# Optimization experiments

Hardware: AMD Instinct MI355X
Metric: run time of the kernel (lower is better)

## Reference

```python
import jax, jax.numpy as jnp
import numpy as np

G = 10            # int(2 / 0.2) BEV grid side
NUM_PILLARS = G * G
INTERVAL = 0.2
BN_EPS = 1e-5


def setup_inputs() -> dict:
    key = jax.random.key(0)
    ks = jax.random.split(key, 8)
    B, N = 8, 20000
    x = jax.random.normal(ks[0], (B, N, 3), dtype=jnp.float32)
    # Linear weights stored as [in, out] (torch Linear applies x @ W.T); no biases.
    W1 = jax.random.normal(ks[1], (6, 32), dtype=jnp.float32) * 0.1
    W2 = jax.random.normal(ks[2], (32, 64), dtype=jnp.float32) * 0.1
    W3 = jax.random.normal(ks[3], (64, 128), dtype=jnp.float32) * 0.1
    W4 = jax.random.normal(ks[4], (256, 768), dtype=jnp.float32) * 0.05
    bn_gamma = jnp.ones((NUM_PILLARS,), dtype=jnp.float32)
    bn_beta = jnp.zeros((NUM_PILLARS,), dtype=jnp.float32)
    return {"x": x, "W1": W1, "W2": W2, "W3": W3, "W4": W4,
            "bn_gamma": bn_gamma, "bn_beta": bn_beta}


def _encode_sample(p, seg, W1, W2, W3, W4):
    # p: [N,3] swapped coords (Z,Y,X); seg: [N] pillar id in [0,100)
    N = p.shape[0]
    counts = jax.ops.segment_sum(jnp.ones((N,), p.dtype), seg, num_segments=NUM_PILLARS)  # [100]
    cent = jax.ops.segment_sum(p, seg, num_segments=NUM_PILLARS) / jnp.maximum(counts, 1.0)[:, None]
    aug = jnp.concatenate([p, p - cent[seg]], axis=-1)          # [N,6]
    h = jax.nn.relu(aug @ W1)
    h = jax.nn.relu(h @ W2)
    h = jax.nn.relu(h @ W3)                                      # [N,128]
    pil = jax.ops.segment_max(h, seg, num_segments=NUM_PILLARS)  # [100,128] (-inf on empty, never gathered)
    h2 = jnp.concatenate([h, pil[seg]], axis=-1)                 # [N,256]
    h2 = jax.nn.relu(h2 @ W4)                                    # [N,768]
    enc = jax.ops.segment_max(h2, seg, num_segments=NUM_PILLARS) # [100,768]
    return jnp.where(counts[:, None] > 0, enc, 0.0)             # empty pillars stay zero


def reference(x, W1, W2, W3, W4, bn_gamma, bn_beta):
    # column swap [Y,Z,X] -> [Z,Y,X]
    pts = jnp.stack([x[..., 1], x[..., 0], x[..., 2]], axis=-1)  # [B,N,3]
    # pillar indices from (Y, X) = swapped cols 1:3
    yx = jnp.clip(pts[..., 1:] + 1.0, 0.0, 1.99)
    idx = jnp.floor(yx / INTERVAL).astype(jnp.int32)             # trunc == floor (non-negative)
    seg = idx[..., 0] * G + idx[..., 1]                          # [B,N], matches flatten(2) order y*10+x
    feat = jax.vmap(lambda p, s: _encode_sample(p, s, W1, W2, W3, W4))(pts, seg)  # [B,100,768]
    # BatchNorm1d(100) in training mode over [B, 100, 768]: stats over dims (0,2)
    mean = feat.mean(axis=(0, 2))
    var = feat.var(axis=(0, 2))  # biased variance, as torch uses for normalization
    out = (feat - mean[None, :, None]) * jax.lax.rsqrt(var + BN_EPS)[None, :, None]
    return out * bn_gamma[None, :, None] + bn_beta[None, :, None]
```

## Files before the change

### kernel.cpp

```cpp
#include <hip/hip_runtime.h>
#include <stdint.h>

#define B_    8
#define N_    20000
#define NPTS  (B_*N_)
#define G_    10
#define NPIL  100
#define NSB   (B_*NPIL)
#define BN_EPS 1e-5f

#define OFF_COUNTS   0
#define OFF_SUMS     3200
#define OFF_STARTS   12800
#define OFF_ZPAD     16064
#define ZERO_BYTES   16320
#define OFF_CENT     19264
#define OFF_SEG      28864
#define OFF_W3BF     668864
#define OFF_W4T      709824
#define OFF_PILBF    1103040
#define OFF_PILW4B   1307840
#define OFF_H3P      3765440
#define WS_NEED      44725440

typedef __attribute__((ext_vector_type(8))) short bf16x8;
typedef __attribute__((ext_vector_type(4))) float f32x4;

typedef const __attribute__((address_space(1))) void gas_void;
typedef __attribute__((address_space(3))) void las_void;

__device__ __forceinline__ void gload_lds16(const void* g, void* l){
    __builtin_amdgcn_global_load_lds((gas_void*)g, (las_void*)l, 16, 0, 0);
}

__device__ __forceinline__ int binidx(float v){
    float t = v + 1.0f;
    t = fminf(fmaxf(t, 0.0f), 1.99f);
    return (int)(t / 0.2f);
}
__device__ __forceinline__ unsigned short f2bf(float f){
    unsigned u = __float_as_uint(f);
    u += 0x7fffu + ((u >> 16) & 1u);
    return (unsigned short)(u >> 16);
}
__device__ __forceinline__ unsigned u16max2(unsigned a, unsigned b){
    unsigned ah=a>>16, bh=b>>16, al=a&0xffffu, bl=b&0xffffu;
    return ((ah>bh?ah:bh)<<16) | (al>bl?al:bl);
}
__device__ __forceinline__ uint4 max16(uint4 a, uint4 b){
    uint4 r; r.x=u16max2(a.x,b.x); r.y=u16max2(a.y,b.y);
    r.z=u16max2(a.z,b.z); r.w=u16max2(a.w,b.w); return r;
}

__global__ __launch_bounds__(256) void kA(const float* __restrict__ x,
                                          int* __restrict__ segrank,
                                          int* __restrict__ counts,
                                          float* __restrict__ sums){
    __shared__ int   lc[NSB];
    __shared__ float lsum[NSB*3];
    __shared__ int   lbase[NSB];
    int tid = threadIdx.x;
    for (int j = tid; j < NSB; j += 256){
        lc[j] = 0;
        lsum[3*j] = 0.f; lsum[3*j+1] = 0.f; lsum[3*j+2] = 0.f;
    }
    __syncthreads();
    int i0 = blockIdx.x * 625;
    int sbv[3], lrv[3];
    #pragma unroll
    for (int t = 0; t < 3; t++){
        int i = i0 + tid + t*256;
        sbv[t] = -1;
        if (tid + t*256 < 625 && i < NPTS){
            float x0 = x[3*i], x1 = x[3*i+1], x2 = x[3*i+2];
            int b  = i / N_;
            int sb = b*NPIL + binidx(x0)*G_ + binidx(x2);
            sbv[t] = sb;
            lrv[t] = atomicAdd(&lc[sb], 1);
            atomicAdd(&lsum[sb*3+0], x1);
            atomicAdd(&lsum[sb*3+1], x0);
            atomicAdd(&lsum[sb*3+2], x2);
        }
    }
    __syncthreads();
    for (int j = tid; j < NSB; j += 256){
        int c = lc[j];
        if (c > 0){
            lbase[j] = atomicAdd(&counts[j], c);
            atomicAdd(&sums[3*j+0], lsum[3*j+0]);
            atomicAdd(&sums[3*j+1], lsum[3*j+1]);
            atomicAdd(&sums[3*j+2], lsum[3*j+2]);
        }
    }
    __syncthreads();
    #pragma unroll
    for (int t = 0; t < 3; t++){
        if (sbv[t] >= 0){
            int i = i0 + tid + t*256;
            int rank = lbase[sbv[t]] + lrv[t];
            segrank[i] = sbv[t] | (rank << 10);
        }
    }
}

__global__ __launch_bounds__(1024) void kScan(const int* __restrict__ counts,
                                              int* __restrict__ starts){
    __shared__ int s[1024];
    int t = threadIdx.x;
    int c = (t < NSB) ? counts[t] : 0;
    s[t] = c;
    __syncthreads();
    for (int off=1; off<1024; off<<=1){
        int v = (t >= off) ? s[t-off] : 0;
        __syncthreads();
        s[t] += v;
        __syncthreads();
    }
    if (t < NSB) starts[t] = s[t]-c;
    if (t == NSB) starts[NSB] = s[NSB-1];
}

__global__ __launch_bounds__(256) void kB(const int* __restrict__ counts,
                                          const float* __restrict__ sums,
                                          float* __restrict__ cent,
                                          const float* __restrict__ W3,
                                          unsigned short* __restrict__ W3bf,
                                          const float* __restrict__ W4,
                                          unsigned short* __restrict__ W4T){
    int idx = blockIdx.x*256 + threadIdx.x;
    if (idx < 2400){
        cent[idx] = sums[idx] / fmaxf((float)counts[idx/3], 1.0f);
    } else if (idx < 2400 + 8192){
        int t = idx - 2400;
        int col = t >> 6, k = t & 63;
        W3bf[t] = f2bf(W3[k*128 + col]);
    } else if (idx < 2400 + 8192 + 196608){
        int t = idx - 2400 - 8192;
        int k = t / 768, j = t - k*768;
        W4T[j*256 + k] = f2bf(W4[t]);
    }
}

__global__ __launch_bounds__(256) void kC12(const float* __restrict__ x,
                                            const int* __restrict__ segrank,
                                            const int* __restrict__ starts,
                                            const float* __restrict__ cent,
                                            const float* __restrict__ W1,
                                            const float* __restrict__ W2,
                                            unsigned short* __restrict__ h3p){
    int i = blockIdx.x*256 + threadIdx.x;
    if (i >= NPTS) return;
    int pk = segrank[i];
    int sb = pk & 1023;
    int pos = starts[sb] + (pk >> 10);
    float p0 = x[3*i+1], p1 = x[3*i], p2 = x[3*i+2];
    float aug[6];
    aug[0]=p0; aug[1]=p1; aug[2]=p2;
    aug[3]=p0-cent[sb*3+0]; aug[4]=p1-cent[sb*3+1]; aug[5]=p2-cent[sb*3+2];

    float h1[32];
    #pragma unroll
    for (int j=0;j<32;j++){
        float a = 0.f;
        #pragma unroll
        for (int k=0;k<6;k++) a += aug[k]*W1[k*32+j];
        h1[j] = fmaxf(a, 0.f);
    }
    unsigned buf[32];
    #pragma unroll 8
    for (int jp=0;jp<32;jp++){
        float a0 = 0.f, a1 = 0.f;
        #pragma unroll
        for (int k=0;k<32;k++){
            a0 += h1[k]*W2[k*64 + jp*2];
            a1 += h1[k]*W2[k*64 + jp*2 + 1];
        }
        buf[jp] = (unsigned)f2bf(fmaxf(a0,0.f)) | ((unsigned)f2bf(fmaxf(a1,0.f)) << 16);
    }
    uint4* d4 = (uint4*)(h3p + (size_t)pos*128 + 64);
    #pragma unroll
    for (int q=0;q<8;q++) d4[q] = ((const uint4*)buf)[q];
}

__global__ __launch_bounds__(512) void kC3(const unsigned short* __restrict__ W3bf,
                                           unsigned short* __restrict__ h3p){
    __shared__ unsigned short Al[256*64];
    __shared__ unsigned short Bl[128*64];
    int tid = threadIdx.x;
    int m0  = blockIdx.x * 256;
    #pragma unroll
    for (int it=0; it<4; it++){
        int cc = tid + it*512;
        int row = cc >> 3, ch = cc & 7;
        int chs = ch ^ (row & 7);
        gload_lds16(h3p + (size_t)(m0+row)*128 + 64 + chs*8, (char*)Al + cc*16);
    }
    #pragma unroll
    for (int it=0; it<2; it++){
        int cc = tid + it*512;
        int row = cc >> 3, ch = cc & 7;
        int chs = ch ^ (row & 7);
        gload_lds16(W3bf + (size_t)row*64 + chs*8, (char*)Bl + cc*16);
    }
    __syncthreads();

    int lane = tid & 63, wid = tid >> 6;
    int wm = wid >> 1, wn = wid & 1;
    int l15 = lane & 15, lhi = lane >> 4;

    f32x4 acc[4][4];
    #pragma unroll
    for (int m=0;m<4;m++)
        #pragma unroll
        for (int n=0;n<4;n++) acc[m][n] = (f32x4){0.f,0.f,0.f,0.f};

    #pragma unroll
    for (int kk=0; kk<2; kk++){
        bf16x8 af[4], bfr[4];
        #pragma unroll
        for (int f=0; f<4; f++){
            int ra = wm*64 + f*16 + l15;
            af[f]  = *(const bf16x8*)((char*)Al + ra*128 + (((kk*4+lhi) ^ (ra&7))*16));
            int rb = wn*64 + f*16 + l15;
            bfr[f] = *(const bf16x8*)((char*)Bl + rb*128 + (((kk*4+lhi) ^ (rb&7))*16));
        }
        #pragma unroll
        for (int m=0;m<4;m++)
            #pragma unroll
            for (int n=0;n<4;n++)
                acc[m][n] = __builtin_amdgcn_mfma_f32_16x16x32_bf16(af[m], bfr[n], acc[m][n], 0,0,0);
    }

    #pragma unroll
    for (int m=0;m<4;m++)
        #pragma unroll
        for (int r=0;r<4;r++){
            int row = m0 + wm*64 + m*16 + lhi*4 + r;
            #pragma unroll
            for (int n=0;n<4;n++){
                int col = wn*64 + n*16 + l15;
                h3p[(size_t)row*128 + col] = f2bf(fmaxf(acc[m][n][r], 0.f));
            }
        }
}

__global__ __launch_bounds__(256) void kM(const unsigned short* __restrict__ h3p,
                                          const int* __restrict__ starts,
                                          unsigned short* __restrict__ pilbf){
    __shared__ uint4 sd[16][16];
    int sb = blockIdx.x;
    int tx = threadIdx.x & 15, ty = threadIdx.x >> 4;
    int s = starts[sb], npts = starts[sb+1] - s;
    uint4 acc = {0u,0u,0u,0u};
    for (int p = ty; p < npts; p += 16){
        uint4 v = *(const uint4*)(h3p + (size_t)(s+p)*128 + tx*8);
        acc = max16(acc, v);
    }
    sd[ty][tx] = acc;
    __syncthreads();
    #pragma unroll
    for (int off=8; off; off>>=1){
        if (ty < off) sd[ty][tx] = max16(sd[ty][tx], sd[ty+off][tx]);
        __syncthreads();
    }
    if (ty == 0) *(uint4*)(pilbf + sb*128 + tx*8) = sd[0][tx];
}

__global__ __launch_bounds__(256) void kPB(const unsigned short* __restrict__ pilbf,
                                           const unsigned short* __restrict__ W4T,
                                           float* __restrict__ pilW4b){
    __shared__ unsigned short Al[128*128];
    __shared__ unsigned short Bl[128*128];
    int m0 = blockIdx.x * 128;
    int n0 = blockIdx.y * 128;
    int tid = threadIdx.x;
    #pragma unroll
    for (int it=0; it<8; it++){
        int cc = tid + it*256;
        int row = cc >> 4, ch = cc & 15;
        int chs = ch ^ (row & 7);
        uint4 v = {0u,0u,0u,0u};
        if (m0 + row < NSB) v = *(const uint4*)(pilbf + (size_t)(m0+row)*128 + chs*8);
        *(uint4*)((char*)Al + cc*16) = v;
        uint4 vb = *(const uint4*)(W4T + (size_t)(n0+row)*256 + 128 + chs*8);
        *(uint4*)((char*)Bl + cc*16) = vb;
    }
    __syncthreads();
    int lane = tid & 63, wid = tid >> 6;
    int wm = wid >> 1, wn = wid & 1;
    int l15 = lane & 15, lhi = lane >> 4;
    f32x4 acc[4][4];
    #pragma unroll
    for (int m=0;m<4;m++)
        #pragma unroll
        for (int n=0;n<4;n++) acc[m][n] = (f32x4){0.f,0.f,0.f,0.f};
    #pragma unroll
    for (int kk=0; kk<4; kk++){
        bf16x8 af[4], bfr[4];
        #pragma unroll
        for (int f=0; f<4; f++){
            int ra = wm*64 + f*16 + l15;
            af[f]  = *(const bf16x8*)((char*)Al + ra*256 + (((kk*4+lhi) ^ (ra&7))*16));
            int rb = wn*64 + f*16 + l15;
            bfr[f] = *(const bf16x8*)((char*)Bl + rb*256 + (((kk*4+lhi) ^ (rb&7))*16));
        }
        #pragma unroll
        for (int m=0;m<4;m++)
            #pragma unroll
            for (int n=0;n<4;n++)
                acc[m][n] = __builtin_amdgcn_mfma_f32_16x16x32_bf16(af[m], bfr[n], acc[m][n], 0,0,0);
    }
    #pragma unroll
    for (int m=0;m<4;m++)
        #pragma unroll
        for (int r=0;r<4;r++){
            int p = wm*64 + m*16 + lhi*4 + r;
            int sbp = m0 + p;
            if (sbp < NSB){
                #pragma unroll
                for (int n=0;n<4;n++)
                    pilW4b[(size_t)sbp*768 + n0 + wn*64 + n*16 + l15] = acc[m][n][r];
            }
        }
}

__global__ __launch_bounds__(256) void kD(const unsigned short* __restrict__ h3p,
                                          const unsigned short* __restrict__ zpad,
                                          const int* __restrict__ starts,
                                          const float* __restrict__ pilW4b,
                                          const unsigned short* __restrict__ W4T,
                                          float* __restrict__ out){
    __shared__ unsigned short Al[64*128];
    __shared__ unsigned short Bl[128*128];
    __shared__ float red[2][2][64];
    int b  = blockIdx.x;
    int x_ = b & 7, t_ = b >> 3;
    int k_ = t_ / 6, nt = t_ - k_*6;
    int sb = x_ + 8*k_;
    int n0 = nt * 128;
    int tid = threadIdx.x;
    int start = starts[sb];
    int npts  = starts[sb+1] - start;
    if (npts == 0){
        if (tid < 128) out[(size_t)sb*768 + n0 + tid] = 0.f;
        return;
    }
    #pragma unroll
    for (int it=0; it<8; it++){
        int cc = tid + it*256;
        int row = cc >> 4, ch = cc & 15;
        int chs = ch ^ (row & 7);
        gload_lds16(W4T + (size_t)(n0+row)*256 + chs*8, (char*)Bl + cc*16);
    }
    int lane = tid & 63, wid = tid >> 6;
    int wm = wid >> 1, wn = wid & 1;
    int l15 = lane & 15, lhi = lane >> 4;

    float mx[2][4][4];
    #pragma unroll
    for (int m=0;m<2;m++)
        #pragma unroll
        for (int n=0;n<4;n++)
            #pragma unroll
            for (int r=0;r<4;r++) mx[m][n][r] = -3.0e38f;

    int nch = (npts + 63) >> 6;
    for (int c=0; c<nch; c++){
        int base = c*64;
        __syncthreads();
        #pragma unroll
        for (int it=0; it<4; it++){
            int cc = tid + it*256;
            int row = cc >> 4, ch = cc & 15;
            int chs = ch ^ (row & 7);
            const unsigned short* src = (base + row < npts)
                ? h3p + (size_t)(start+base+row)*128 + chs*8
                : zpad + chs*8;
            gload_lds16(src, (char*)Al + cc*16);
        }
        __syncthreads();

        f32x4 acc[2][4];
        #pragma unroll
        for (int m=0;m<2;m++)
            #pragma unroll
            for (int n=0;n<4;n++) acc[m][n] = (f32x4){0.f,0.f,0.f,0.f};

        #pragma unroll
        for (int kk=0; kk<4; kk++){
            bf16x8 af[2], bfr[4];
            #pragma unroll
            for (int f=0; f<2; f++){
                int ra = wm*32 + f*16 + l15;
                af[f]  = *(const bf16x8*)((char*)Al + ra*256 + (((kk*4+lhi) ^ (ra&7))*16));
            }
            #pragma unroll
            for (int f=0; f<4; f++){
                int rb = wn*64 + f*16 + l15;
                bfr[f] = *(const bf16x8*)((char*)Bl + rb*256 + (((kk*4+lhi) ^ (rb&7))*16));
            }
            #pragma unroll
            for (int m=0;m<2;m++)
                #pragma unroll
                for (int n=0;n<4;n++)
                    acc[m][n] = __builtin_amdgcn_mfma_f32_16x16x32_bf16(af[m], bfr[n], acc[m][n], 0,0,0);
        }

        int nrem = npts - base;
        #pragma unroll
        for (int m=0;m<2;m++)
            #pragma unroll
            for (int r=0;r<4;r++){
                int p = wm*32 + m*16 + lhi*4 + r;
                if (p < nrem){
                    #pragma unroll
                    for (int n=0;n<4;n++)
                        mx[m][n][r] = fmaxf(mx[m][n][r], acc[m][n][r]);
                }
            }
    }

    float red4[4];
    #pragma unroll
    for (int n=0;n<4;n++){
        float v = -3.0e38f;
        #pragma unroll
        for (int m=0;m<2;m++)
            #pragma unroll
            for (int r=0;r<4;r++) v = fmaxf(v, mx[m][n][r]);
        v = fmaxf(v, __shfl_xor(v, 16));
        v = fmaxf(v, __shfl_xor(v, 32));
        red4[n] = v;
    }
    if (lhi == 0){
        #pragma unroll
        for (int n=0;n<4;n++) red[wm][wn][n*16 + l15] = red4[n];
    }
    __syncthreads();
    if (wm == 0){
        float v = fmaxf(red[0][wn][lane], red[1][wn][lane]);
        int col = n0 + wn*64 + lane;
        v = fmaxf(v + pilW4b[(size_t)sb*768 + col], 0.f);
        out[(size_t)sb*768 + col] = v;
    }
}

__global__ __launch_bounds__(256) void kE(float* __restrict__ out,
                                          const float* __restrict__ gamma,
                                          const float* __restrict__ beta){
    int p = blockIdx.x;
    int tid = threadIdx.x;
    float v[B_*3];
    float sum = 0.f, ssq = 0.f;
    #pragma unroll
    for (int b=0;b<B_;b++)
        #pragma unroll
        for (int r=0;r<3;r++){
            float t = out[(b*NPIL + p)*768 + tid + r*256];
            v[b*3+r] = t;
            sum += t; ssq += t*t;
        }
    #pragma unroll
    for (int off=32; off; off>>=1){
        sum += __shfl_xor(sum, off);
        ssq += __shfl_xor(ssq, off);
    }
    __shared__ float ls[8];
    __shared__ float sc[2];
    int lane = tid & 63, w = tid >> 6;
    if (lane == 0){ ls[w] = sum; ls[4+w] = ssq; }
    __syncthreads();
    if (tid == 0){
        float S = ls[0]+ls[1]+ls[2]+ls[3];
        float Q = ls[4]+ls[5]+ls[6]+ls[7];
        float mean = S * (1.0f/6144.0f);
        float var  = Q * (1.0f/6144.0f) - mean*mean;
        float scale = rsqrtf(var + BN_EPS) * gamma[p];
        sc[0] = scale;
        sc[1] = beta[p] - mean*scale;
    }
    __syncthreads();
    float scale = sc[0], shift = sc[1];
    #pragma unroll
    for (int b=0;b<B_;b++)
        #pragma unroll
        for (int r=0;r<3;r++)
            out[(b*NPIL + p)*768 + tid + r*256] = v[b*3+r]*scale + shift;
}

extern "C" void kernel_launch(void* const* d_in, const int* in_sizes, int n_in,
                              void* d_out, int out_size, void* d_ws, size_t ws_size,
                              hipStream_t stream){
    if (ws_size < (size_t)WS_NEED) return;
    const float* x     = (const float*)d_in[0];
    const float* W1    = (const float*)d_in[1];
    const float* W2    = (const float*)d_in[2];
    const float* W3    = (const float*)d_in[3];
    const float* W4    = (const float*)d_in[4];
    const float* gamma = (const float*)d_in[5];
    const float* beta  = (const float*)d_in[6];
    float* out = (float*)d_out;
    char*  ws  = (char*)d_ws;

    int*            counts = (int*)           (ws + OFF_COUNTS);
    float*          sums   = (float*)         (ws + OFF_SUMS);
    int*            starts = (int*)           (ws + OFF_STARTS);
    unsigned short* zpad   = (unsigned short*)(ws + OFF_ZPAD);
    float*          cent   = (float*)         (ws + OFF_CENT);
    int*            segrank= (int*)           (ws + OFF_SEG);
    unsigned short* W3bf   = (unsigned short*)(ws + OFF_W3BF);
    unsigned short* W4T    = (unsigned short*)(ws + OFF_W4T);
    unsigned short* pilbf  = (unsigned short*)(ws + OFF_PILBF);
    float*          pilW4b = (float*)         (ws + OFF_PILW4B);
    unsigned short* h3p    = (unsigned short*)(ws + OFF_H3P);

    hipMemsetAsync(d_ws, 0, ZERO_BYTES, stream);

    kA<<<256, 256, 0, stream>>>(x, segrank, counts, sums);
    kScan<<<1, 1024, 0, stream>>>(counts, starts);
    kB<<<(2400+8192+196608+255)/256, 256, 0, stream>>>(counts, sums, cent, W3, W3bf, W4, W4T);
    kC12<<<(NPTS+255)/256, 256, 0, stream>>>(x, segrank, starts, cent, W1, W2, h3p);
    kC3<<<NPTS/256, 512, 0, stream>>>(W3bf, h3p);
    kM<<<NSB, 256, 0, stream>>>(h3p, starts, pilbf);
    dim3 gPB((NSB+127)/128, 6);
    kPB<<<gPB, 256, 0, stream>>>(pilbf, W4T, pilW4b);
    kD<<<4800, 256, 0, stream>>>(h3p, zpad, starts, pilW4b, W4T, out);
    kE<<<NPIL, 256, 0, stream>>>(out, gamma, beta);
}
```

Baseline: 173.1 us.

## Split kD into full-chunk fast path and masked tail, widen LDS swizzle

kD's point loop now treats full 64-row chunks separately. They use precomputed, pointer-incremented source addresses with no zero-pad selection and no per-row masking in the max. Only the last partial chunk clamps its indices and masks rows. The LDS XOR swizzle is widened from 3 to 4 bits in kD and kPB to cut bank conflicts on MFMA fragment reads. kA now uses 100 per-batch pillar bins in shared memory instead of 800, since each 625-point block falls in a single batch.

```diff
diff --git a/kernel.cpp b/kernel.cpp
--- a/kernel.cpp
+++ b/kernel.cpp
@@ -12,7 +12,6 @@
 #define OFF_COUNTS   0
 #define OFF_SUMS     3200
 #define OFF_STARTS   12800
-#define OFF_ZPAD     16064
 #define ZERO_BYTES   16320
 #define OFF_CENT     19264
 #define OFF_SEG      28864
@@ -52,53 +51,77 @@
     r.z=u16max2(a.z,b.z); r.w=u16max2(a.w,b.w); return r;
 }
 
+__device__ __forceinline__ void kd_mfma(const unsigned short* Al, const unsigned short* Bl,
+                                        int wm, int wn, int l15, int lhi, f32x4 acc[2][4]){
+    #pragma unroll
+    for (int kk=0; kk<4; kk++){
+        bf16x8 af[2], bfr[4];
+        #pragma unroll
+        for (int f=0; f<2; f++){
+            int ra = wm*32 + f*16 + l15;
+            af[f]  = *(const bf16x8*)((const char*)Al + ra*256 + (((kk*4+lhi) ^ (ra&15))*16));
+        }
+        #pragma unroll
+        for (int f=0; f<4; f++){
+            int rb = wn*64 + f*16 + l15;
+            bfr[f] = *(const bf16x8*)((const char*)Bl + rb*256 + (((kk*4+lhi) ^ (rb&15))*16));
+        }
+        #pragma unroll
+        for (int m=0;m<2;m++)
+            #pragma unroll
+            for (int n=0;n<4;n++)
+                acc[m][n] = __builtin_amdgcn_mfma_f32_16x16x32_bf16(af[m], bfr[n], acc[m][n], 0,0,0);
+    }
+}
+
 __global__ __launch_bounds__(256) void kA(const float* __restrict__ x,
                                           int* __restrict__ segrank,
                                           int* __restrict__ counts,
                                           float* __restrict__ sums){
-    __shared__ int   lc[NSB];
-    __shared__ float lsum[NSB*3];
-    __shared__ int   lbase[NSB];
+    __shared__ int   lc[NPIL];
+    __shared__ float lsum[NPIL*3];
+    __shared__ int   lbase[NPIL];
     int tid = threadIdx.x;
-    for (int j = tid; j < NSB; j += 256){
-        lc[j] = 0;
-        lsum[3*j] = 0.f; lsum[3*j+1] = 0.f; lsum[3*j+2] = 0.f;
-    }
-    __syncthreads();
-    int i0 = blockIdx.x * 625;
-    int sbv[3], lrv[3];
+    if (tid < NPIL){
+        lc[tid] = 0;
+        lsum[3*tid] = 0.f; lsum[3*tid+1] = 0.f; lsum[3*tid+2] = 0.f;
+    }
+    __syncthreads();
+    int i0  = blockIdx.x * 625;
+    int bat = i0 / N_;
+    int sv[3], lrv[3];
     #pragma unroll
     for (int t = 0; t < 3; t++){
-        int i = i0 + tid + t*256;
-        sbv[t] = -1;
-        if (tid + t*256 < 625 && i < NPTS){
+        int ii = tid + t*256;
+        int i  = i0 + ii;
+        sv[t] = -1;
+        if (ii < 625){
             float x0 = x[3*i], x1 = x[3*i+1], x2 = x[3*i+2];
-            int b  = i / N_;
-            int sb = b*NPIL + binidx(x0)*G_ + binidx(x2);
-            sbv[t] = sb;
-            lrv[t] = atomicAdd(&lc[sb], 1);
-            atomicAdd(&lsum[sb*3+0], x1);
-            atomicAdd(&lsum[sb*3+1], x0);
-            atomicAdd(&lsum[sb*3+2], x2);
-        }
-    }
-    __syncthreads();
-    for (int j = tid; j < NSB; j += 256){
-        int c = lc[j];
+            int s = binidx(x0)*G_ + binidx(x2);
+            sv[t] = s;
+            lrv[t] = atomicAdd(&lc[s], 1);
+            atomicAdd(&lsum[s*3+0], x1);
+            atomicAdd(&lsum[s*3+1], x0);
+            atomicAdd(&lsum[s*3+2], x2);
+        }
+    }
+    __syncthreads();
+    if (tid < NPIL){
+        int c = lc[tid];
         if (c > 0){
-            lbase[j] = atomicAdd(&counts[j], c);
-            atomicAdd(&sums[3*j+0], lsum[3*j+0]);
-            atomicAdd(&sums[3*j+1], lsum[3*j+1]);
-            atomicAdd(&sums[3*j+2], lsum[3*j+2]);
+            int sb = bat*NPIL + tid;
+            lbase[tid] = atomicAdd(&counts[sb], c);
+            atomicAdd(&sums[3*sb+0], lsum[3*tid+0]);
+            atomicAdd(&sums[3*sb+1], lsum[3*tid+1]);
+            atomicAdd(&sums[3*sb+2], lsum[3*tid+2]);
         }
     }
     __syncthreads();
     #pragma unroll
     for (int t = 0; t < 3; t++){
-        if (sbv[t] >= 0){
+        if (sv[t] >= 0){
             int i = i0 + tid + t*256;
-            int rank = lbase[sbv[t]] + lrv[t];
-            segrank[i] = sbv[t] | (rank << 10);
+            segrank[i] = (bat*NPIL + sv[t]) | ((lbase[sv[t]] + lrv[t]) << 10);
         }
     }
 }
@@ -278,7 +301,7 @@
     for (int it=0; it<8; it++){
         int cc = tid + it*256;
         int row = cc >> 4, ch = cc & 15;
-        int chs = ch ^ (row & 7);
+        int chs = ch ^ (row & 15);
         uint4 v = {0u,0u,0u,0u};
         if (m0 + row < NSB) v = *(const uint4*)(pilbf + (size_t)(m0+row)*128 + chs*8);
         *(uint4*)((char*)Al + cc*16) = v;
@@ -300,9 +323,9 @@
         #pragma unroll
         for (int f=0; f<4; f++){
             int ra = wm*64 + f*16 + l15;
-            af[f]  = *(const bf16x8*)((char*)Al + ra*256 + (((kk*4+lhi) ^ (ra&7))*16));
+            af[f]  = *(const bf16x8*)((char*)Al + ra*256 + (((kk*4+lhi) ^ (ra&15))*16));
             int rb = wn*64 + f*16 + l15;
-            bfr[f] = *(const bf16x8*)((char*)Bl + rb*256 + (((kk*4+lhi) ^ (rb&7))*16));
+            bfr[f] = *(const bf16x8*)((char*)Bl + rb*256 + (((kk*4+lhi) ^ (rb&15))*16));
         }
         #pragma unroll
         for (int m=0;m<4;m++)
@@ -325,7 +348,6 @@
 }
 
 __global__ __launch_bounds__(256) void kD(const unsigned short* __restrict__ h3p,
-                                          const unsigned short* __restrict__ zpad,
                                           const int* __restrict__ starts,
                                           const float* __restrict__ pilW4b,
                                           const unsigned short* __restrict__ W4T,
@@ -349,8 +371,18 @@
     for (int it=0; it<8; it++){
         int cc = tid + it*256;
         int row = cc >> 4, ch = cc & 15;
-        int chs = ch ^ (row & 7);
+        int chs = ch ^ (row & 15);
         gload_lds16(W4T + (size_t)(n0+row)*256 + chs*8, (char*)Bl + cc*16);
+    }
+    const unsigned short* asrc[4];
+    int arow[4];
+    #pragma unroll
+    for (int it=0; it<4; it++){
+        int cc = tid + it*256;
+        int row = cc >> 4, ch = cc & 15;
+        int chs = ch ^ (row & 15);
+        arow[it] = row;
+        asrc[it] = h3p + (size_t)(start+row)*128 + chs*8;
     }
     int lane = tid & 63, wid = tid >> 6;
     int wm = wid >> 1, wn = wid & 1;
@@ -364,55 +396,55 @@
             #pragma unroll
             for (int r=0;r<4;r++) mx[m][n][r] = -3.0e38f;
 
-    int nch = (npts + 63) >> 6;
-    for (int c=0; c<nch; c++){
-        int base = c*64;
+    int nfull = npts >> 6;
+    int tailr = npts - (nfull << 6);
+
+    for (int c=0; c<nfull; c++){
         __syncthreads();
         #pragma unroll
         for (int it=0; it<4; it++){
+            gload_lds16(asrc[it], (char*)Al + (tid + it*256)*16);
+            asrc[it] += 64*128;
+        }
+        __syncthreads();
+        f32x4 acc[2][4];
+        #pragma unroll
+        for (int m=0;m<2;m++)
+            #pragma unroll
+            for (int n=0;n<4;n++) acc[m][n] = (f32x4){0.f,0.f,0.f,0.f};
+        kd_mfma(Al, Bl, wm, wn, l15, lhi, acc);
+        #pragma unroll
+        for (int m=0;m<2;m++)
+            #pragma unroll
+            for (int n=0;n<4;n++)
+                #pragma unroll
+                for (int r=0;r<4;r++)
+                    mx[m][n][r] = fmaxf(mx[m][n][r], acc[m][n][r]);
+    }
+    if (tailr > 0){
+        int base = nfull << 6;
+        __syncthreads();
+        #pragma unroll
+        for (int it=0; it<4; it++){
+            int idx = start + base + arow[it];
+            idx = idx < NPTS ? idx : NPTS-1;
             int cc = tid + it*256;
-            int row = cc >> 4, ch = cc & 15;
-            int chs = ch ^ (row & 7);
-            const unsigned short* src = (base + row < npts)
-                ? h3p + (size_t)(start+base+row)*128 + chs*8
-                : zpad + chs*8;
-            gload_lds16(src, (char*)Al + cc*16);
-        }
-        __syncthreads();
-
+            int chs = (cc & 15) ^ (arow[it] & 15);
+            gload_lds16(h3p + (size_t)idx*128 + chs*8, (char*)Al + cc*16);
+        }
+        __syncthreads();
         f32x4 acc[2][4];
         #pragma unroll
         for (int m=0;m<2;m++)
             #pragma unroll
             for (int n=0;n<4;n++) acc[m][n] = (f32x4){0.f,0.f,0.f,0.f};
-
-        #pragma unroll
-        for (int kk=0; kk<4; kk++){
-            bf16x8 af[2], bfr[4];
-            #pragma unroll
-            for (int f=0; f<2; f++){
-                int ra = wm*32 + f*16 + l15;
-                af[f]  = *(const bf16x8*)((char*)Al + ra*256 + (((kk*4+lhi) ^ (ra&7))*16));
-            }
-            #pragma unroll
-            for (int f=0; f<4; f++){
-                int rb = wn*64 + f*16 + l15;
-                bfr[f] = *(const bf16x8*)((char*)Bl + rb*256 + (((kk*4+lhi) ^ (rb&7))*16));
-            }
-            #pragma unroll
-            for (int m=0;m<2;m++)
-                #pragma unroll
-                for (int n=0;n<4;n++)
-                    acc[m][n] = __builtin_amdgcn_mfma_f32_16x16x32_bf16(af[m], bfr[n], acc[m][n], 0,0,0);
-        }
-
-        int nrem = npts - base;
+        kd_mfma(Al, Bl, wm, wn, l15, lhi, acc);
         #pragma unroll
         for (int m=0;m<2;m++)
             #pragma unroll
             for (int r=0;r<4;r++){
                 int p = wm*32 + m*16 + lhi*4 + r;
-                if (p < nrem){
+                if (p < tailr){
                     #pragma unroll
                     for (int n=0;n<4;n++)
                         mx[m][n][r] = fmaxf(mx[m][n][r], acc[m][n][r]);
@@ -505,7 +537,6 @@
     int*            counts = (int*)           (ws + OFF_COUNTS);
     float*          sums   = (float*)         (ws + OFF_SUMS);
     int*            starts = (int*)           (ws + OFF_STARTS);
-    unsigned short* zpad   = (unsigned short*)(ws + OFF_ZPAD);
     float*          cent   = (float*)         (ws + OFF_CENT);
     int*            segrank= (int*)           (ws + OFF_SEG);
     unsigned short* W3bf   = (unsigned short*)(ws + OFF_W3BF);
@@ -524,6 +555,6 @@
     kM<<<NSB, 256, 0, stream>>>(h3p, starts, pilbf);
     dim3 gPB((NSB+127)/128, 6);
     kPB<<<gPB, 256, 0, stream>>>(pilbf, W4T, pilW4b);
-    kD<<<4800, 256, 0, stream>>>(h3p, zpad, starts, pilW4b, W4T, out);
+    kD<<<4800, 256, 0, stream>>>(h3p, starts, pilW4b, W4T, out);
     kE<<<NPIL, 256, 0, stream>>>(out, gamma, beta);
 }
```

After: 164.5 us, median of 2. 5.0% less time.
